# Performance work log

Measured on AMD Instinct MI355X. Metric: run time of the kernel, lower is better.

## Reference

```python
import jax, jax.numpy as jnp
import numpy as np

B, T, E, H, L = 16, 512, 768, 12, 100
D = E // H
LN_EPS = 1e-12
NEG = -1e9


def setup_inputs() -> dict:
    key = jax.random.key(0)
    ks = jax.random.split(key, 12)
    s = 1.0 / np.sqrt(E)
    inp = {
        "last_hidden_states": jax.random.normal(ks[0], (B, T, E), jnp.float32),
        "att_mask": jnp.ones((B, T), jnp.float32),
        "type_emb": jax.random.normal(ks[1], (L, E), jnp.float32),
        # learned params
        "tp": jax.random.normal(ks[2], (E,), jnp.float32),
        "Wq": jax.random.normal(ks[3], (E, E), jnp.float32) * s,
        "bq": jnp.zeros((E,), jnp.float32),
        "Wk": jax.random.normal(ks[4], (E, E), jnp.float32) * s,
        "bk": jnp.zeros((E,), jnp.float32),
        "Wv": jax.random.normal(ks[5], (E, E), jnp.float32) * s,
        "bv": jnp.zeros((E,), jnp.float32),
        "Wo": jax.random.normal(ks[6], (E, E), jnp.float32) * s,
        "bo": jnp.zeros((E,), jnp.float32),
        "ln_g": jnp.ones((E,), jnp.float32),
        "ln_b": jnp.zeros((E,), jnp.float32),
    }
    return inp


def _layer_norm(x, g, b):
    mu = x.mean(-1, keepdims=True)
    var = ((x - mu) ** 2).mean(-1, keepdims=True)
    return (x - mu) * jax.lax.rsqrt(var + LN_EPS) * g + b


def reference(last_hidden_states, att_mask, type_emb, tp,
              Wq, bq, Wk, bk, Wv, bv, Wo, bo, ln_g, ln_b):
    b, t, e = last_hidden_states.shape
    # --- label cross-attention (no head split, no scaling) ---
    scores = jnp.einsum('bte,le->btl', last_hidden_states, type_emb)      # [b,t,l]
    att = jax.nn.softmax(scores, axis=-1)
    first_label_emb = jnp.einsum('btl,le->bte', att, type_emb)            # [b,t,e]

    h_truth = last_hidden_states + first_label_emb
    h_unknown = last_hidden_states + tp                                   # broadcast tp over [b,t]

    # --- two-stream masked self-attention: Q from unknown, K/V from truth,
    #     each position masked from attending to its own truth state ---
    q = (h_unknown @ Wq + bq).reshape(b, t, H, D)
    k = (h_truth @ Wk + bk).reshape(b, t, H, D)
    v = (h_truth @ Wv + bv).reshape(b, t, H, D)
    logits = jnp.einsum('bqhd,bkhd->bhqk', q, k) / np.sqrt(D).astype(np.float32)
    pad_bias = (1.0 - att_mask)[:, None, None, :] * NEG                   # [b,1,1,t]
    diag_bias = jnp.eye(t, dtype=logits.dtype)[None, None] * NEG          # [1,1,t,t]
    probs = jax.nn.softmax(logits + pad_bias + diag_bias, axis=-1)
    ctx = jnp.einsum('bhqk,bkhd->bqhd', probs, v).reshape(b, t, e)
    attn_out = ctx @ Wo + bo
    twice_hidden = _layer_norm(attn_out + h_unknown, ln_g, ln_b)

    out = twice_hidden + last_hidden_states + first_label_emb
    return out, scores
```

## Files before the change

### kernel.cpp

```cpp
#include <hip/hip_runtime.h>

typedef unsigned char u8;
typedef unsigned short u16;
typedef u16 u16x4 __attribute__((ext_vector_type(4)));
typedef u16 u16x8 __attribute__((ext_vector_type(8)));
typedef __bf16 bf16x8 __attribute__((ext_vector_type(8)));
typedef float f32x2 __attribute__((ext_vector_type(2)));
typedef float f32x4 __attribute__((ext_vector_type(4)));
typedef long longx2 __attribute__((ext_vector_type(2)));

#define BB 16
#define TT 512
#define EE 768
#define HH 12
#define DD 64
#define LL 100
#define BT (BB*TT)
#define BTE ((size_t)BT*EE)
#define LOG2E 1.44269504f
#define QSCALE (0.125f*LOG2E)
#define FIXMAX 44.0f
#define PSTR 72

__device__ __forceinline__ float bf2f(u16 u){
  union { float f; unsigned int i; } v; v.i = ((unsigned int)u) << 16; return v.f;
}
__device__ __forceinline__ u16 f2bf(float f){
  __bf16 h = (__bf16)f;
  union { __bf16 h; u16 u; } v; v.h = h; return v.u;
}
__device__ __forceinline__ u16 pk_fp8(float a, float b){
  return (u16)(__builtin_amdgcn_cvt_pk_fp8_f32(a, b, 0, false) & 0xffff);
}
__device__ __forceinline__ u8 f2fp8(float a){
  return (u8)(__builtin_amdgcn_cvt_pk_fp8_f32(a, 0.f, 0, false) & 0xff);
}

__device__ __forceinline__ void gload16(const void* g, void* l){
  __builtin_amdgcn_global_load_lds(
      (const __attribute__((address_space(1))) void*)g,
      (__attribute__((address_space(3))) void*)l, 16, 0, 0);
}

__global__ __launch_bounds__(256,1) void prep_all_kernel(
    const float* __restrict__ Wq, const float* __restrict__ Wk,
    const float* __restrict__ Wv, const float* __restrict__ Wo,
    u8* __restrict__ WT8,
    const float* __restrict__ TE, u16* __restrict__ TEb, u16* __restrict__ TEt,
    const float* __restrict__ mask, float* __restrict__ MBg)
{
  __shared__ float tile[64][65];
  int bx = blockIdx.x;
  int tid = threadIdx.x;
  if (bx < 576){
    int m  = bx / 144, t = bx % 144;
    int tr = t / 12,  tc = t % 12;
    const float* W = (m==0)?Wq : (m==1)?Wk : (m==2)?Wv : Wo;
    u8* dst = WT8 + (size_t)m * EE * EE;
#pragma unroll
    for (int i=0;i<16;i++){
      int idx = tid + 256*i; int r = idx>>6, c = idx&63;
      tile[r][c] = W[(size_t)(tr*64+r)*EE + tc*64 + c];
    }
    __syncthreads();
#pragma unroll
    for (int i=0;i<8;i++){
      int idx = tid + 256*i;
      int r = idx >> 5, cp = idx & 31;
      u16 pk = pk_fp8(tile[cp*2][r], tile[cp*2+1][r]);
      *(u16*)&dst[(size_t)(tc*64+r)*EE + tr*64 + cp*2] = pk;
    }
  } else if (bx < 960){
    int e = (bx - 576)*2 + (tid >> 7);
    int c = tid & 127;
    u16 v = 0;
    if (c < LL) v = f2bf(TE[(size_t)c*EE + e]);
    TEt[(size_t)e*128 + c] = v;
    if (e < 128){
#pragma unroll
      for (int k=c; k<EE; k+=128)
        TEb[(size_t)e*EE + k] = (e < LL) ? f2bf(TE[(size_t)e*EE + k]) : (u16)0;
    }
  } else {
    int i = (bx - 960)*256 + tid;
    MBg[i] = (1.0f - mask[i]) * (-1e9f * LOG2E) - FIXMAX;
  }
}

__global__ __launch_bounds__(64) void label_scores_kernel(
    const float* __restrict__ X, const u16* __restrict__ TEb,
    float* __restrict__ scores_out, u16* __restrict__ att)
{
  int m0 = blockIdx.x * 16;
  int lane = threadIdx.x;
  int l15 = lane & 15, g = lane >> 4;

  const float* xrow = X + (size_t)(m0 + l15)*EE;
  f32x4 s[7] = {};
  for (int k0=0; k0<EE; k0+=64){
    bf16x8 af[2];
#pragma unroll
    for (int kk=0;kk<2;kk++){
      const float* src = xrow + k0 + kk*32 + g*8;
      float4 a = *(const float4*)src, b = *(const float4*)(src+4);
      bf16x8 o;
      o[0]=(__bf16)a.x; o[1]=(__bf16)a.y; o[2]=(__bf16)a.z; o[3]=(__bf16)a.w;
      o[4]=(__bf16)b.x; o[5]=(__bf16)b.y; o[6]=(__bf16)b.z; o[7]=(__bf16)b.w;
      af[kk] = o;
    }
#pragma unroll
    for (int nt=0;nt<7;nt++){
      bf16x8 b0 = *(const bf16x8*)&TEb[(size_t)(nt*16+l15)*EE + k0 + g*8];
      bf16x8 b1 = *(const bf16x8*)&TEb[(size_t)(nt*16+l15)*EE + k0 + 32 + g*8];
      s[nt] = __builtin_amdgcn_mfma_f32_16x16x32_bf16(af[0], b0, s[nt], 0,0,0);
      s[nt] = __builtin_amdgcn_mfma_f32_16x16x32_bf16(af[1], b1, s[nt], 0,0,0);
    }
  }

  int rowb = m0 + g*4;
#pragma unroll
  for (int nt=0;nt<7;nt++){
    int col = nt*16 + l15;
    if (col < LL){
#pragma unroll
      for (int r=0;r<4;r++)
        scores_out[(size_t)(rowb + r)*LL + col] = s[nt][r];
    }
  }
  if (l15 >= 4){
#pragma unroll
    for (int r=0;r<4;r++) s[6][r] = -1e30f;
  }
  float inv[4];
#pragma unroll
  for (int r=0;r<4;r++){
    float tm = s[0][r];
#pragma unroll
    for (int nt=1;nt<7;nt++) tm = fmaxf(tm, s[nt][r]);
    tm = fmaxf(tm, __shfl_xor(tm, 1, 16));
    tm = fmaxf(tm, __shfl_xor(tm, 2, 16));
    tm = fmaxf(tm, __shfl_xor(tm, 4, 16));
    tm = fmaxf(tm, __shfl_xor(tm, 8, 16));
    float ps = 0.f;
#pragma unroll
    for (int nt=0;nt<7;nt++){
      float p = exp2f((s[nt][r] - tm) * LOG2E);
      s[nt][r] = p; ps += p;
    }
    ps += __shfl_xor(ps, 1, 16);
    ps += __shfl_xor(ps, 2, 16);
    ps += __shfl_xor(ps, 4, 16);
    ps += __shfl_xor(ps, 8, 16);
    inv[r] = 1.f/ps;
  }
#pragma unroll
  for (int nt=0;nt<7;nt++){
    int col = nt*16 + l15;
#pragma unroll
    for (int r=0;r<4;r++)
      att[(size_t)(rowb + r)*128 + col] = f2bf(s[nt][r] * inv[r]);
  }
  {
    int col = 112 + l15;
#pragma unroll
    for (int r=0;r<4;r++) att[(size_t)(rowb + r)*128 + col] = 0;
  }
}

__global__ __launch_bounds__(256,1) void gemm_fle_kernel(
    const u16* __restrict__ A, const u16* __restrict__ BTw,
    const float* __restrict__ Xf, const float* __restrict__ tp,
    u8* __restrict__ HT8, u8* __restrict__ HU8, int N, int K)
{
  __shared__ u16 As[128*40];
  __shared__ u16 Bs[128*40];
  int nb = N >> 7;
  int m0 = (blockIdx.x / nb) << 7;
  int n0 = (blockIdx.x % nb) << 7;
  int tid  = threadIdx.x, lane = tid & 63, w = tid >> 6;
  int wm = (w >> 1) << 6, wn = (w & 1) << 6;
  int lr = lane & 15, lk = (lane >> 4) << 3;

  f32x4 acc[4][4] = {};

  for (int k0 = 0; k0 < K; k0 += 32){
    __syncthreads();
#pragma unroll
    for (int i=0;i<2;i++){
      int idx = tid + (i<<8);
      int row = idx >> 2, kq = (idx & 3) << 3;
      *(u16x8*)&As[row*40 + kq] = *(const u16x8*)&A  [(size_t)(m0+row)*K + k0 + kq];
      *(u16x8*)&Bs[row*40 + kq] = *(const u16x8*)&BTw[(size_t)(n0+row)*K + k0 + kq];
    }
    __syncthreads();
    bf16x8 af[4], bfr[4];
#pragma unroll
    for (int i=0;i<4;i++) af [i] = *(const bf16x8*)&As[(wm + i*16 + lr)*40 + lk];
#pragma unroll
    for (int j=0;j<4;j++) bfr[j] = *(const bf16x8*)&Bs[(wn + j*16 + lr)*40 + lk];
#pragma unroll
    for (int i=0;i<4;i++)
#pragma unroll
      for (int j=0;j<4;j++)
        acc[i][j] = __builtin_amdgcn_mfma_f32_16x16x32_bf16(af[i], bfr[j], acc[i][j], 0, 0, 0);
  }

  int rbase = (lane >> 4) << 2;
#pragma unroll
  for (int j=0;j<4;j++){
    int col = n0 + wn + j*16 + lr;
    float tpv = tp[col];
#pragma unroll
    for (int i=0;i<4;i++){
#pragma unroll
      for (int r=0;r<4;r++){
        int row = m0 + wm + i*16 + rbase + r;
        float x = Xf[(size_t)row*EE + col];
        HT8[(size_t)row*EE + col] = f2fp8(x + acc[i][j][r]);
        HU8[(size_t)row*EE + col] = f2fp8(x + tpv);
      }
    }
  }
}

template<int NB, int FUSED>
__global__ __launch_bounds__(256,2) void gemm8_kernel(
    const u8* __restrict__ A0, const u8* __restrict__ A1,
    const u8* __restrict__ Wb,
    const float* __restrict__ b0, const float* __restrict__ b1,
    const float* __restrict__ b2,
    u16* __restrict__ C0, u16* __restrict__ C1, u16* __restrict__ C2)
{
  __shared__ __align__(16) u8 smem[33792];
  u8* As = smem;
  u8* Bs = smem + 16384;
  u16* Cs = (u16*)smem;
  const int K = EE;

  int nwg = gridDim.x;
  int bid = blockIdx.x;
  int cpx = nwg >> 3;
  int swz = (bid & 7) * cpx + (bid >> 3);
  int mb = swz / NB, nb = swz % NB;
  int m0 = mb << 7;
  int n0 = (FUSED ? (nb % 6) : nb) << 7;

  int which = FUSED ? (nb / 6) : 0;
  const u8* Ap; const u8* Wp; const float* bp; u16* Cp;
  if (!FUSED){ Ap = A0; Wp = Wb; bp = b0; Cp = C0; }
  else {
    if (which == 0){ Ap = A0; Wp = Wb;                      bp = b0; Cp = C0; }
    else if (which == 1){ Ap = A1; Wp = Wb + (size_t)EE*EE; bp = b1; Cp = C1; }
    else { Ap = A1; Wp = Wb + 2*(size_t)EE*EE;              bp = b2; Cp = C2; }
  }

  int tid = threadIdx.x, lane = tid & 63, w = tid >> 6;
  int wm = (w >> 1) << 6, wn = (w & 1) << 6;
  int lr = lane & 15, g = lane >> 4;
  int lrow = lane >> 3;
  int lchunk = (lane & 7) ^ lrow;

  f32x4 acc[4][4] = {};

  for (int k0 = 0; k0 < K; k0 += 128){
    __syncthreads();
#pragma unroll
    for (int t=0;t<4;t++){
      int r0 = w*32 + t*8;
      gload16(&Ap[(size_t)(m0 + r0 + lrow)*K + k0 + (lchunk<<4)], &As[r0*128]);
      gload16(&Wp[(size_t)(n0 + r0 + lrow)*K + k0 + (lchunk<<4)], &Bs[r0*128]);
    }
    __syncthreads();
#pragma unroll
    for (int t=0;t<2;t++){
      int cs = ((t<<2) + g) ^ (lr & 7);
      longx2 af[4], bfr[4];
#pragma unroll
      for (int i=0;i<4;i++) af [i] = *(const longx2*)&As[(wm + i*16 + lr)*128 + (cs<<4)];
#pragma unroll
      for (int j=0;j<4;j++) bfr[j] = *(const longx2*)&Bs[(wn + j*16 + lr)*128 + (cs<<4)];
#pragma unroll
      for (int i=0;i<4;i++)
#pragma unroll
        for (int j=0;j<4;j++){
          acc[i][j] = __builtin_amdgcn_mfma_f32_16x16x32_fp8_fp8(af[i][0], bfr[j][0], acc[i][j], 0, 0, 0);
          acc[i][j] = __builtin_amdgcn_mfma_f32_16x16x32_fp8_fp8(af[i][1], bfr[j][1], acc[i][j], 0, 0, 0);
        }
    }
  }

  int rbase = (lane >> 4) << 2;
  float scq = (FUSED && which==0) ? QSCALE : 1.0f;
  __syncthreads();
#pragma unroll
  for (int j=0;j<4;j++){
    int col = wn + j*16 + lr;
    float bv = bp[n0 + col];
#pragma unroll
    for (int i=0;i<4;i++)
#pragma unroll
      for (int r=0;r<4;r++)
        Cs[(wm + i*16 + rbase + r)*132 + col] = f2bf((acc[i][j][r] + bv) * scq);
  }
  __syncthreads();

  if (FUSED && which == 2){
    int bb = m0 >> 9, t0 = m0 & 511;
    int colb = tid >> 2;
    int tq = (tid & 3) << 3;
#pragma unroll
    for (int c2=0;c2<2;c2++){
      int col = colb + (c2<<6);
      int hh = (n0 + col) >> 6, d = (n0 + col) & 63;
      u16* dst = &Cp[((size_t)(bb*HH + hh)*DD + d)*TT + t0];
#pragma unroll
      for (int s=0;s<4;s++){
        int tt = tq + (s<<5);
        u16x8 v;
#pragma unroll
        for (int e=0;e<8;e++) v[e] = Cs[(tt+e)*132 + col];
        *(u16x8*)&dst[tt] = v;
      }
    }
  } else {
#pragma unroll
    for (int p=0;p<2;p++){
      int row = (tid >> 2) + (p<<6);
      int c0 = (tid & 3) << 3;
      size_t gbase = (size_t)(m0 + row)*EE + n0;
      const u16* src = &Cs[row*132];
#pragma unroll
      for (int s=0;s<4;s++){
        int c = c0 + (s<<5);
        u16x4 lo = *(const u16x4*)&src[c];
        u16x4 hi = *(const u16x4*)&src[c+4];
        u16x8 v;
#pragma unroll
        for (int e=0;e<4;e++){ v[e] = lo[e]; v[e+4] = hi[e]; }
        *(u16x8*)&Cp[gbase + c] = v;
      }
    }
  }
}

__global__ __launch_bounds__(256,3) void attn_mfma_kernel(
    const u16* __restrict__ Q, const u16* __restrict__ K,
    const u16* __restrict__ VT, const float* __restrict__ MBg,
    u8* __restrict__ CTX8)
{
  __shared__ u16 Ks [2][64*64];
  __shared__ u16 VTs[2][64*64];
  __shared__ u16 Pl [4][32*PSTR];

  int bx = blockIdx.x;
  int bh = bx % (BB*HH), q0 = (bx / (BB*HH)) << 7;
  int b = bh / HH, h = bh % HH;
  int tid = threadIdx.x, lane = tid & 63, w = tid >> 6;
  int l15 = lane & 15, g = lane >> 4;
  int wq0 = q0 + w*32;
  size_t rowbase = (size_t)b*TT;
  u16* pw = &Pl[w][0];
  const u16* Kbh = K  + rowbase*EE + h*DD;
  const u16* Vbh = VT + (size_t)bh*DD*TT;
  int lrow = lane >> 3, lchunk = (lane & 7) ^ (lane >> 3);

  bf16x8 qf[2][2];
#pragma unroll
  for (int i=0;i<2;i++)
#pragma unroll
    for (int kk=0;kk<2;kk++)
      qf[i][kk] = *(const bf16x8*)&Q[(rowbase + wq0 + i*16 + l15)*EE + h*DD + kk*32 + g*8];

  f32x4 ctxf[2][4] = {};
  float lrun[2][4] = {};

#define STAGE(buf, k0)                                                          \
  { _Pragma("unroll")                                                           \
    for (int it=0; it<2; ++it){                                                 \
      int r0 = w*16 + it*8;                                                     \
      gload16(&Kbh[(size_t)((k0) + r0 + lrow)*EE + (lchunk<<3)], &Ks [buf][r0*64]); \
      gload16(&Vbh[(size_t)(r0 + lrow)*TT + (k0) + (lchunk<<3)], &VTs[buf][r0*64]); } }

  STAGE(0, 0);

  for (int kt=0; kt<8; ++kt){
    int k0 = kt << 6;
    int buf = kt & 1;
    __syncthreads();

    float mb[4];
#pragma unroll
    for (int kb=0;kb<4;kb++) mb[kb] = MBg[rowbase + k0 + kb*16 + l15];

    if (kt < 7) STAGE(buf^1, k0+64);

    f32x4 s[2][4] = {};
#pragma unroll
    for (int kk=0;kk<2;kk++){
      int cs = ((kk<<2) + g) ^ (l15 & 7);
      bf16x8 kf[4];
#pragma unroll
      for (int kb=0;kb<4;kb++)
        kf[kb] = *(const bf16x8*)&Ks[buf][(kb*16 + l15)*64 + (cs<<3)];
#pragma unroll
      for (int i=0;i<2;i++)
#pragma unroll
        for (int kb=0;kb<4;kb++)
          s[i][kb] = __builtin_amdgcn_mfma_f32_16x16x32_bf16(qf[i][kk], kf[kb], s[i][kb], 0,0,0);
    }

    if ((k0 < wq0 + 32) && (k0 + 64 > wq0)){
#pragma unroll
      for (int i=0;i<2;i++){
        int qr = wq0 + i*16 + g*4;
#pragma unroll
        for (int kb=0;kb<4;kb++){
          int kpos = k0 + kb*16 + l15;
#pragma unroll
          for (int r=0;r<4;r++)
            if (kpos == qr + r) s[i][kb][r] -= 1e9f*LOG2E;
        }
      }
    }

#pragma unroll
    for (int i=0;i<2;i++)
#pragma unroll
      for (int kb=0;kb<4;kb++)
#pragma unroll
        for (int r=0;r<4;r++){
          float p = exp2f(s[i][kb][r] + mb[kb]);
          lrun[i][r] += p;
          pw[(i*16 + g*4 + r)*PSTR + kb*16 + l15] = f2bf(p);
        }

    bf16x8 pa[2][2];
#pragma unroll
    for (int i=0;i<2;i++)
#pragma unroll
      for (int kk=0;kk<2;kk++)
        pa[i][kk] = *(const bf16x8*)&pw[(i*16 + l15)*PSTR + kk*32 + g*8];

#pragma unroll
    for (int kk=0;kk<2;kk++){
      int cs = ((kk<<2) + g) ^ (l15 & 7);
      bf16x8 vf[4];
#pragma unroll
      for (int dj=0;dj<4;dj++)
        vf[dj] = *(const bf16x8*)&VTs[buf][(dj*16 + l15)*64 + (cs<<3)];
#pragma unroll
      for (int i=0;i<2;i++)
#pragma unroll
        for (int dj=0;dj<4;dj++)
          ctxf[i][dj] = __builtin_amdgcn_mfma_f32_16x16x32_bf16(pa[i][kk], vf[dj], ctxf[i][dj], 0,0,0);
    }
  }
#undef STAGE

  float inv[2][4];
#pragma unroll
  for (int i=0;i<2;i++)
#pragma unroll
    for (int r=0;r<4;r++){
      float l = lrun[i][r];
      l += __shfl_xor(l, 1, 16);
      l += __shfl_xor(l, 2, 16);
      l += __shfl_xor(l, 4, 16);
      l += __shfl_xor(l, 8, 16);
      inv[i][r] = 1.0f / l;
    }
#pragma unroll
  for (int i=0;i<2;i++)
#pragma unroll
    for (int dj=0;dj<4;dj++)
#pragma unroll
      for (int r=0;r<4;r++)
        pw[(i*16 + g*4 + r)*64 + dj*16 + l15] = f2bf(ctxf[i][dj][r] * inv[i][r]);
#pragma unroll
  for (int t=0;t<4;t++){
    int row = lane >> 1, c = ((lane & 1)<<5) + t*8;
    const u16* pv = &pw[row*64 + c];
    u16x4 o8;
#pragma unroll
    for (int e=0;e<4;e++) o8[e] = pk_fp8(bf2f(pv[2*e]), bf2f(pv[2*e+1]));
    *(u16x4*)&CTX8[(rowbase + wq0 + row)*EE + h*DD + c] = o8;
  }
}

__global__ __launch_bounds__(192,1) void ln_out_kernel(
    const u16* __restrict__ AO, const u8* __restrict__ HU8,
    const u8* __restrict__ HT8, const float* __restrict__ g,
    const float* __restrict__ bta, float* __restrict__ out)
{
  __shared__ float red[3];
  int r = blockIdx.x, tid = threadIdx.x;
  size_t base = (size_t)r*EE;
  int e0 = tid*4;
  u16x4 ao = *(const u16x4*)&AO[base+e0];
  int hu4 = *(const int*)&HU8[base+e0];
  int ht4 = *(const int*)&HT8[base+e0];
  f32x2 hulo = __builtin_amdgcn_cvt_pk_f32_fp8(hu4, false);
  f32x2 huhi = __builtin_amdgcn_cvt_pk_f32_fp8(hu4, true);
  f32x2 htlo = __builtin_amdgcn_cvt_pk_f32_fp8(ht4, false);
  f32x2 hthi = __builtin_amdgcn_cvt_pk_f32_fp8(ht4, true);
  float huv[4] = {hulo[0], hulo[1], huhi[0], huhi[1]};
  float htv[4] = {htlo[0], htlo[1], hthi[0], hthi[1]};
  float x[4];
#pragma unroll
  for (int j=0;j<4;j++) x[j] = bf2f(ao[j]) + huv[j];

  float s = x[0]+x[1]+x[2]+x[3];
#pragma unroll
  for (int o=32;o;o>>=1) s += __shfl_xor(s, o, 64);
  int w = tid>>6;
  if ((tid&63)==0) red[w] = s;
  __syncthreads();
  float mu = (red[0]+red[1]+red[2]) * (1.0f/EE);
  __syncthreads();
  float d2 = 0.f;
#pragma unroll
  for (int j=0;j<4;j++){ float d = x[j]-mu; d2 += d*d; }
#pragma unroll
  for (int o=32;o;o>>=1) d2 += __shfl_xor(d2, o, 64);
  if ((tid&63)==0) red[w] = d2;
  __syncthreads();
  float var = (red[0]+red[1]+red[2]) * (1.0f/EE);
  float rs = rsqrtf(var + 1e-12f);
  float4 gg = *(const float4*)&g[e0];
  float4 bb = *(const float4*)&bta[e0];
  float4 o4;
  o4.x = (x[0]-mu)*rs*gg.x + bb.x + htv[0];
  o4.y = (x[1]-mu)*rs*gg.y + bb.y + htv[1];
  o4.z = (x[2]-mu)*rs*gg.z + bb.z + htv[2];
  o4.w = (x[3]-mu)*rs*gg.w + bb.w + htv[3];
  *(float4*)&out[base+e0] = o4;
}

extern "C" void kernel_launch(void* const* d_in, const int* in_sizes, int n_in,
                              void* d_out, int out_size, void* d_ws, size_t ws_size,
                              hipStream_t stream)
{
  (void)in_sizes; (void)n_in; (void)out_size; (void)ws_size;
  const float* X    = (const float*)d_in[0];
  const float* mask = (const float*)d_in[1];
  const float* TE   = (const float*)d_in[2];
  const float* tp   = (const float*)d_in[3];
  const float* Wq   = (const float*)d_in[4];
  const float* bq   = (const float*)d_in[5];
  const float* Wk   = (const float*)d_in[6];
  const float* bk   = (const float*)d_in[7];
  const float* Wv   = (const float*)d_in[8];
  const float* bv   = (const float*)d_in[9];
  const float* Wo   = (const float*)d_in[10];
  const float* bo   = (const float*)d_in[11];
  const float* ln_g = (const float*)d_in[12];
  const float* ln_b = (const float*)d_in[13];

  float* out    = (float*)d_out;
  float* scores = out + BTE;

  char* p = (char*)d_ws;
  u8*  HT8  = (u8*)p;  p += BTE;
  u8*  HU8  = (u8*)p;  p += BTE;
  u8*  CTX8 = (u8*)p;  p += BTE;
  u8*  WT8  = (u8*)p;  p += (size_t)4*EE*EE;
  u16* Qb   = (u16*)p; p += BTE*2;
  u16* Kb   = (u16*)p; p += BTE*2;
  u16* VTb  = (u16*)p; p += BTE*2;
  u16* AOb  = (u16*)p; p += BTE*2;
  u16* ATT  = (u16*)p; p += (size_t)BT*128*2;
  u16* TEb  = (u16*)p; p += (size_t)128*EE*2;
  u16* TEt  = (u16*)p; p += (size_t)EE*128*2;
  float* MBg = (float*)p;

  prep_all_kernel<<<dim3(992), dim3(256), 0, stream>>>(
      Wq, Wk, Wv, Wo, WT8, TE, TEb, TEt, mask, MBg);

  label_scores_kernel<<<dim3(BT/16), dim3(64), 0, stream>>>(X, TEb, scores, ATT);

  gemm_fle_kernel<<<dim3((BT/128)*(EE/128)), dim3(256), 0, stream>>>(
      ATT, TEt, X, tp, HT8, HU8, EE, 128);

  gemm8_kernel<18,1><<<dim3(64*18), dim3(256), 0, stream>>>(
      HU8, HT8, WT8, bq, bk, bv, Qb, Kb, VTb);

  attn_mfma_kernel<<<dim3(BB*HH*4), dim3(256), 0, stream>>>(Qb, Kb, VTb, MBg, CTX8);

  gemm8_kernel<6,0><<<dim3(64*6), dim3(256), 0, stream>>>(
      CTX8, nullptr, WT8 + 3*(size_t)EE*EE, bo, nullptr, nullptr, AOb, nullptr, nullptr);

  ln_out_kernel<<<dim3(BT), dim3(192), 0, stream>>>(AOb, HU8, HT8, ln_g, ln_b, out);
}
```

Measured before the change: 114.6 us.

## Store Q and K in FP8 and use FP8 MFMA for attention scores

The fused QKV GEMM now writes Q and K as packed FP8 instead of bf16. The attention kernel loads them with a new swizzled LDS layout and computes QK^T with the fp8 16x16x32 MFMA. This halves the Q/K write and read traffic and the K LDS footprint. In exchange, the attention logits lose precision, and the Q scale folded into the values interacts with FP8 range.

```diff
diff --git a/kernel.cpp b/kernel.cpp
--- a/kernel.cpp
+++ b/kernel.cpp
@@ -229,7 +229,7 @@
     const u8* __restrict__ Wb,
     const float* __restrict__ b0, const float* __restrict__ b1,
     const float* __restrict__ b2,
-    u16* __restrict__ C0, u16* __restrict__ C1, u16* __restrict__ C2)
+    void* C0v, void* C1v, void* C2v)
 {
   __shared__ __align__(16) u8 smem[33792];
   u8* As = smem;
@@ -246,12 +246,12 @@
   int n0 = (FUSED ? (nb % 6) : nb) << 7;
 
   int which = FUSED ? (nb / 6) : 0;
-  const u8* Ap; const u8* Wp; const float* bp; u16* Cp;
-  if (!FUSED){ Ap = A0; Wp = Wb; bp = b0; Cp = C0; }
+  const u8* Ap; const u8* Wp; const float* bp;
+  if (!FUSED){ Ap = A0; Wp = Wb; bp = b0; }
   else {
-    if (which == 0){ Ap = A0; Wp = Wb;                      bp = b0; Cp = C0; }
-    else if (which == 1){ Ap = A1; Wp = Wb + (size_t)EE*EE; bp = b1; Cp = C1; }
-    else { Ap = A1; Wp = Wb + 2*(size_t)EE*EE;              bp = b2; Cp = C2; }
+    if (which == 0){ Ap = A0; Wp = Wb;                      bp = b0; }
+    else if (which == 1){ Ap = A1; Wp = Wb + (size_t)EE*EE; bp = b1; }
+    else { Ap = A1; Wp = Wb + 2*(size_t)EE*EE;              bp = b2; }
   }
 
   int tid = threadIdx.x, lane = tid & 63, w = tid >> 6;
@@ -305,6 +305,7 @@
   __syncthreads();
 
   if (FUSED && which == 2){
+    u16* Cp = (u16*)C2v;
     int bb = m0 >> 9, t0 = m0 & 511;
     int colb = tid >> 2;
     int tq = (tid & 3) << 3;
@@ -322,7 +323,8 @@
         *(u16x8*)&dst[tt] = v;
       }
     }
-  } else {
+  } else if (FUSED){
+    u8* Cp8 = (u8*)(which==0 ? C0v : C1v);
 #pragma unroll
     for (int p=0;p<2;p++){
       int row = (tid >> 2) + (p<<6);
@@ -334,6 +336,27 @@
         int c = c0 + (s<<5);
         u16x4 lo = *(const u16x4*)&src[c];
         u16x4 hi = *(const u16x4*)&src[c+4];
+        u16x4 o8;
+        o8[0] = pk_fp8(bf2f(lo[0]), bf2f(lo[1]));
+        o8[1] = pk_fp8(bf2f(lo[2]), bf2f(lo[3]));
+        o8[2] = pk_fp8(bf2f(hi[0]), bf2f(hi[1]));
+        o8[3] = pk_fp8(bf2f(hi[2]), bf2f(hi[3]));
+        *(u16x4*)&Cp8[gbase + c] = o8;
+      }
+    }
+  } else {
+    u16* Cp = (u16*)C0v;
+#pragma unroll
+    for (int p=0;p<2;p++){
+      int row = (tid >> 2) + (p<<6);
+      int c0 = (tid & 3) << 3;
+      size_t gbase = (size_t)(m0 + row)*EE + n0;
+      const u16* src = &Cs[row*132];
+#pragma unroll
+      for (int s=0;s<4;s++){
+        int c = c0 + (s<<5);
+        u16x4 lo = *(const u16x4*)&src[c];
+        u16x4 hi = *(const u16x4*)&src[c+4];
         u16x8 v;
 #pragma unroll
         for (int e=0;e<4;e++){ v[e] = lo[e]; v[e+4] = hi[e]; }
@@ -344,11 +367,11 @@
 }
 
 __global__ __launch_bounds__(256,3) void attn_mfma_kernel(
-    const u16* __restrict__ Q, const u16* __restrict__ K,
+    const u8* __restrict__ Q8, const u8* __restrict__ K8,
     const u16* __restrict__ VT, const float* __restrict__ MBg,
     u8* __restrict__ CTX8)
 {
-  __shared__ u16 Ks [2][64*64];
+  __shared__ __align__(16) u8 Ks[2][64*64];
   __shared__ u16 VTs[2][64*64];
   __shared__ u16 Pl [4][32*PSTR];
 
@@ -360,25 +383,28 @@
   int wq0 = q0 + w*32;
   size_t rowbase = (size_t)b*TT;
   u16* pw = &Pl[w][0];
-  const u16* Kbh = K  + rowbase*EE + h*DD;
+  const u8*  Kbh = K8 + rowbase*EE + h*DD;
   const u16* Vbh = VT + (size_t)bh*DD*TT;
   int lrow = lane >> 3, lchunk = (lane & 7) ^ (lane >> 3);
-
-  bf16x8 qf[2][2];
+  int krow = lane >> 2;
+  int kchunk = (lane & 3) ^ ((lane >> 3) & 3);
+
+  long qf8[2][2];
 #pragma unroll
   for (int i=0;i<2;i++)
 #pragma unroll
     for (int kk=0;kk<2;kk++)
-      qf[i][kk] = *(const bf16x8*)&Q[(rowbase + wq0 + i*16 + l15)*EE + h*DD + kk*32 + g*8];
+      qf8[i][kk] = *(const long*)&Q8[(rowbase + wq0 + i*16 + l15)*EE + h*DD + kk*32 + g*8];
 
   f32x4 ctxf[2][4] = {};
   float lrun[2][4] = {};
 
 #define STAGE(buf, k0)                                                          \
-  { _Pragma("unroll")                                                           \
+  { gload16(&Kbh[(size_t)((k0) + w*16 + krow)*EE + (kchunk<<4)],                \
+            &Ks[buf][(w*16)*64]);                                               \
+    _Pragma("unroll")                                                           \
     for (int it=0; it<2; ++it){                                                 \
       int r0 = w*16 + it*8;                                                     \
-      gload16(&Kbh[(size_t)((k0) + r0 + lrow)*EE + (lchunk<<3)], &Ks [buf][r0*64]); \
       gload16(&Vbh[(size_t)(r0 + lrow)*TT + (k0) + (lchunk<<3)], &VTs[buf][r0*64]); } }
 
   STAGE(0, 0);
@@ -395,18 +421,21 @@
     if (kt < 7) STAGE(buf^1, k0+64);
 
     f32x4 s[2][4] = {};
+    int f8 = ((l15 >> 1) & 3) << 1;
 #pragma unroll
     for (int kk=0;kk<2;kk++){
-      int cs = ((kk<<2) + g) ^ (l15 & 7);
-      bf16x8 kf[4];
-#pragma unroll
-      for (int kb=0;kb<4;kb++)
-        kf[kb] = *(const bf16x8*)&Ks[buf][(kb*16 + l15)*64 + (cs<<3)];
+      long kop[4];
+#pragma unroll
+      for (int kb=0;kb<4;kb++){
+        int R = kb*16 + l15;
+        int slot8 = ((kk<<2) + g) ^ f8;
+        kop[kb] = *(const long*)&Ks[buf][R*64 + (slot8<<3)];
+      }
 #pragma unroll
       for (int i=0;i<2;i++)
 #pragma unroll
         for (int kb=0;kb<4;kb++)
-          s[i][kb] = __builtin_amdgcn_mfma_f32_16x16x32_bf16(qf[i][kk], kf[kb], s[i][kb], 0,0,0);
+          s[i][kb] = __builtin_amdgcn_mfma_f32_16x16x32_fp8_fp8(qf8[i][kk], kop[kb], s[i][kb], 0,0,0);
     }
 
     if ((k0 < wq0 + 32) && (k0 + 64 > wq0)){
@@ -564,8 +593,8 @@
   u8*  HU8  = (u8*)p;  p += BTE;
   u8*  CTX8 = (u8*)p;  p += BTE;
   u8*  WT8  = (u8*)p;  p += (size_t)4*EE*EE;
-  u16* Qb   = (u16*)p; p += BTE*2;
-  u16* Kb   = (u16*)p; p += BTE*2;
+  u8*  Qb8  = (u8*)p;  p += BTE;
+  u8*  Kb8  = (u8*)p;  p += BTE;
   u16* VTb  = (u16*)p; p += BTE*2;
   u16* AOb  = (u16*)p; p += BTE*2;
   u16* ATT  = (u16*)p; p += (size_t)BT*128*2;
@@ -582,12 +611,13 @@
       ATT, TEt, X, tp, HT8, HU8, EE, 128);
 
   gemm8_kernel<18,1><<<dim3(64*18), dim3(256), 0, stream>>>(
-      HU8, HT8, WT8, bq, bk, bv, Qb, Kb, VTb);
-
-  attn_mfma_kernel<<<dim3(BB*HH*4), dim3(256), 0, stream>>>(Qb, Kb, VTb, MBg, CTX8);
+      HU8, HT8, WT8, bq, bk, bv, (void*)Qb8, (void*)Kb8, (void*)VTb);
+
+  attn_mfma_kernel<<<dim3(BB*HH*4), dim3(256), 0, stream>>>(Qb8, Kb8, VTb, MBg, CTX8);
 
   gemm8_kernel<6,0><<<dim3(64*6), dim3(256), 0, stream>>>(
-      CTX8, nullptr, WT8 + 3*(size_t)EE*EE, bo, nullptr, nullptr, AOb, nullptr, nullptr);
+      CTX8, nullptr, WT8 + 3*(size_t)EE*EE, bo, nullptr, nullptr,
+      (void*)AOb, nullptr, nullptr);
 
   ln_out_kernel<<<dim3(BT), dim3(192), 0, stream>>>(AOb, HU8, HT8, ln_g, ln_b, out);
 }
```

After: 113.2 us. About the same (-1.3%).
